# Kernel optimization log

Hardware: AMD Instinct MI355X
Metric: run time of the kernel (lower is better)

Reference implementation:

```python
import jax, jax.numpy as jnp
import numpy as np

B, N_PROP = 2, 512
C_FEAT, FH, FW = 256, 200, 200
NUM_CLASSES, NUM_STAGES = 81, 3
POOL, SR, SCALE = 7, 2, 0.25
IMG_H, IMG_W = 800.0, 800.0
FC_DIM = 1024
IN_DIM = C_FEAT * POOL * POOL
STDS = ((0.1, 0.1, 0.2, 0.2), (0.05, 0.05, 0.1, 0.1), (0.033, 0.033, 0.067, 0.067))
CLIP_VAL = float(np.log(1000.0 / 16))
SCORE_T, NMS_T, DETS, PRE_NMS = 0.05, 0.5, 100, 2048


def bilinear(f, y, x):
    # f: [C,H,W]; y,x: [M] sample coords (torchvision roi_align bilinear rules)
    H, W = f.shape[1], f.shape[2]
    valid = (y > -1.0) & (y < H) & (x > -1.0) & (x < W)
    y = jnp.clip(y, 0.0, H - 1.0)
    x = jnp.clip(x, 0.0, W - 1.0)
    y0 = jnp.floor(y).astype(jnp.int32)
    x0 = jnp.floor(x).astype(jnp.int32)
    y1 = jnp.minimum(y0 + 1, H - 1)
    x1 = jnp.minimum(x0 + 1, W - 1)
    ly, lx = y - y0, x - x0
    hy, hx = 1.0 - ly, 1.0 - lx
    v = (hy * hx) * f[:, y0, x0] + (hy * lx) * f[:, y0, x1] \
      + (ly * hx) * f[:, y1, x0] + (ly * lx) * f[:, y1, x1]
    return v * valid  # [C,M]


def roi_align(f, rois):
    # f: [C,H,W], rois: [N,4] image coords -> [N,C,POOL,POOL]
    b = rois * SCALE
    x1, y1, x2, y2 = b[:, 0], b[:, 1], b[:, 2], b[:, 3]
    rw = jnp.maximum(x2 - x1, 1.0)
    rh = jnp.maximum(y2 - y1, 1.0)
    bw, bh = rw / POOL, rh / POOL
    p = jnp.arange(POOL, dtype=f.dtype)
    s = (jnp.arange(SR, dtype=f.dtype) + 0.5) / SR
    gy = y1[:, None, None] + (p[None, :, None] + s[None, None, :]) * bh[:, None, None]  # [N,P,SR]
    gx = x1[:, None, None] + (p[None, :, None] + s[None, None, :]) * bw[:, None, None]
    n = rois.shape[0]
    yy = jnp.broadcast_to(gy[:, :, :, None, None], (n, POOL, SR, POOL, SR))
    xx = jnp.broadcast_to(gx[:, None, None, :, :], (n, POOL, SR, POOL, SR))
    vals = bilinear(f, yy.reshape(-1), xx.reshape(-1))  # [C, N*P*SR*P*SR]
    vals = vals.reshape(f.shape[0], n, POOL, SR, POOL, SR).mean(axis=(3, 5))
    return vals.transpose(1, 0, 2, 3)


def decode_clip(props, deltas, stds):
    px1, py1, px2, py2 = props[:, 0], props[:, 1], props[:, 2], props[:, 3]
    pw = jnp.maximum(px2 - px1, 1e-6)
    ph = jnp.maximum(py2 - py1, 1e-6)
    px = px1 + 0.5 * pw
    py = py1 + 0.5 * ph
    wx, wy, ww, wh = stds
    dx = deltas[:, 0] * wx
    dy = deltas[:, 1] * wy
    dw = jnp.minimum(deltas[:, 2] * ww, CLIP_VAL)
    dh = jnp.minimum(deltas[:, 3] * wh, CLIP_VAL)
    gx = dx * pw + px
    gy = dy * ph + py
    gw = jnp.exp(dw) * pw
    gh = jnp.exp(dh) * ph
    return jnp.stack([jnp.clip(gx - 0.5 * gw, 0.0, IMG_W),
                      jnp.clip(gy - 0.5 * gh, 0.0, IMG_H),
                      jnp.clip(gx + 0.5 * gw, 0.0, IMG_W),
                      jnp.clip(gy + 0.5 * gh, 0.0, IMG_H)], axis=1)


def box_iou(a, b):
    area_a = (a[:, 2] - a[:, 0]) * (a[:, 3] - a[:, 1])
    area_b = (b[:, 2] - b[:, 0]) * (b[:, 3] - b[:, 1])
    lt = jnp.maximum(a[:, None, :2], b[None, :, :2])
    rb = jnp.minimum(a[:, None, 2:], b[None, :, 2:])
    wh = jnp.maximum(rb - lt, 0.0)
    inter = wh[..., 0] * wh[..., 1]
    return inter / (area_a[:, None] + area_b[None, :] - inter + 1e-12)


def postprocess(boxes, probs):
    # boxes [N,4], probs [N,NUM_CLASSES] -> fixed-size padded detections
    n = boxes.shape[0]
    ws = boxes[:, 2] - boxes[:, 0]
    hs = boxes[:, 3] - boxes[:, 1]
    ok = (ws >= 1.0) & (hs >= 1.0)  # remove_small_boxes(min_size=1.0)
    fg = probs[:, 1:]               # drop background (class 0)
    sc = jnp.where((fg > SCORE_T) & ok[:, None], fg, -1.0).reshape(-1)  # [N*(C-1)]
    labels = jnp.broadcast_to(jnp.arange(1, NUM_CLASSES, dtype=jnp.int32)[None, :],
                              (n, NUM_CLASSES - 1)).reshape(-1)
    bflat = jnp.broadcast_to(boxes[:, None, :], (n, NUM_CLASSES - 1, 4)).reshape(-1, 4)
    vals, idx = jax.lax.top_k(sc, PRE_NMS)  # fixed-size candidate cap, sorted desc
    bsel = bflat[idx]
    lsel = labels[idx]
    # batched_nms trick: offset boxes per label so classes never overlap
    off = bsel + (lsel.astype(bsel.dtype) * (jnp.max(bsel) + 1.0))[:, None]
    iou = box_iou(off, off)
    valid = vals > 0.0
    ar = jnp.arange(PRE_NMS)
    def body(i, keep):
        sup = (iou[i] > NMS_T) & keep[i]
        return keep & ~(sup & (ar > i))
    keep = jax.lax.fori_loop(0, PRE_NMS, body, valid)
    order = jnp.argsort(jnp.where(keep, ar, PRE_NMS + ar))[:DETS]  # kept first, score order
    kv = keep[order]
    out_boxes = jnp.where(kv[:, None], bsel[order], 0.0)
    out_scores = jnp.where(kv, vals[order], 0.0)
    out_labels = jnp.where(kv, lsel[order], 0)
    return out_boxes, out_scores, out_labels


def cascade_forward(features, proposals, W1, b1, W2, b2, Wc, bc, Wr, br):
    cur = proposals  # [B,N,4]
    logits = None
    for s in range(NUM_STAGES):
        pooled = jax.vmap(roi_align)(features, cur)  # [B,N,C,P,P]
        x = pooled.reshape(B * N_PROP, IN_DIM)
        h = jax.nn.relu(x @ W1[s] + b1[s])
        h = jax.nn.relu(h @ W2[s] + b2[s])
        logits = h @ Wc[s] + bc[s]
        deltas = (h @ Wr[s] + br[s]).reshape(B, N_PROP, 4)
        stds = STDS[s]
        cur = jax.vmap(lambda p, d: decode_clip(p, d, stds))(cur, deltas)
    probs = jax.nn.softmax(logits, axis=-1).reshape(B, N_PROP, NUM_CLASSES)
    return jax.vmap(postprocess)(cur, probs)


def setup_inputs() -> dict:
    key = jax.random.key(0)
    ks = jax.random.split(key, 12)
    features = jax.random.normal(ks[0], (B, C_FEAT, FH, FW), jnp.float32)
    cx = jax.random.uniform(ks[1], (B, N_PROP), minval=0.0, maxval=IMG_W)
    cy = jax.random.uniform(ks[2], (B, N_PROP), minval=0.0, maxval=IMG_H)
    w = jax.random.uniform(ks[3], (B, N_PROP), minval=16.0, maxval=256.0)
    h = jax.random.uniform(ks[4], (B, N_PROP), minval=16.0, maxval=256.0)
    proposals = jnp.stack([jnp.clip(cx - w / 2, 0.0, IMG_W), jnp.clip(cy - h / 2, 0.0, IMG_H),
                           jnp.clip(cx + w / 2, 0.0, IMG_W), jnp.clip(cy + h / 2, 0.0, IMG_H)],
                          axis=-1)
    def lin(k, fan_in, shape):
        return jax.random.normal(k, shape, jnp.float32) / np.sqrt(fan_in).astype(np.float32)
    W1 = lin(ks[5], IN_DIM, (NUM_STAGES, IN_DIM, FC_DIM))
    W2 = lin(ks[6], FC_DIM, (NUM_STAGES, FC_DIM, FC_DIM))
    Wc = lin(ks[7], FC_DIM, (NUM_STAGES, FC_DIM, NUM_CLASSES))
    Wr = lin(ks[8], FC_DIM, (NUM_STAGES, FC_DIM, 4)) * 0.5
    b1 = jnp.zeros((NUM_STAGES, FC_DIM), jnp.float32)
    b2 = jnp.zeros((NUM_STAGES, FC_DIM), jnp.float32)
    bc = jnp.zeros((NUM_STAGES, NUM_CLASSES), jnp.float32)
    br = jnp.zeros((NUM_STAGES, 4), jnp.float32)
    return {"features": features, "proposals": proposals, "W1": W1, "b1": b1,
            "W2": W2, "b2": b2, "Wc": Wc, "bc": bc, "Wr": Wr, "br": br}


def reference(features, proposals, W1, b1, W2, b2, Wc, bc, Wr, br):
    return cascade_forward(features, proposals, W1, b1, W2, b2, Wc, bc, Wr, br)
```

## Files before the change

### kernel.cpp

```cpp
#include <hip/hip_runtime.h>
#include <float.h>
#include <math.h>

#define NB 2
#define NPROP 512
#define NROI 1024
#define CFEAT 256
#define FH 200
#define FW 200
#define HWSZ 40000
#define INDIM 12544
#define FCD 1024
#define NCLS 81
#define NCAND 40960
#define CAP 4096
#define NSEL 2048
#define DETS 100
#define CLIPV 4.135166556742356f

#define KKT1 392
#define KKT2 32
#define SPLITK 8

typedef __attribute__((ext_vector_type(8))) short short8v;
typedef __attribute__((ext_vector_type(8))) unsigned short ushort8v;
typedef __attribute__((ext_vector_type(4))) float float4v;

__device__ __forceinline__ unsigned short f2bf(float x) {
    unsigned u = __float_as_uint(x);
    unsigned r = (u + 0x7fffu + ((u >> 16) & 1u)) >> 16;
    return (unsigned short)r;
}
__device__ __forceinline__ float bf2f(unsigned short b) {
    return __uint_as_float(((unsigned)b) << 16);
}
__device__ __forceinline__ void split3(float x, unsigned short& h, unsigned short& m, unsigned short& l) {
    h = f2bf(x);
    float r1 = x - bf2f(h);
    m = f2bf(r1);
    float r2 = r1 - bf2f(m);
    l = f2bf(r2);
}

__device__ __forceinline__ void gload_lds16(const void* g, void* l) {
    __builtin_amdgcn_global_load_lds((const __attribute__((address_space(1))) unsigned int*)g,
                                     (__attribute__((address_space(3))) unsigned int*)l, 16, 0, 0);
}

__device__ __forceinline__ int swz8k(int o) {
    return o ^ ((((o >> 6) ^ (o >> 8)) & 3) << 4);
}

__global__ void zero_ints_k(int* p, int n) {
    int i = blockIdx.x * blockDim.x + threadIdx.x;
    if (i < n) p[i] = 0;
}

__global__ __launch_bounds__(256) void transpose_k(const float* __restrict__ in, float* __restrict__ out) {
    __shared__ float tile[32][33];
    int b = blockIdx.z;
    int hw0 = blockIdx.x * 32;
    int c0 = blockIdx.y * 32;
    int tx = threadIdx.x;
    int ty = threadIdx.y;
#pragma unroll
    for (int i = 0; i < 32; i += 8)
        tile[ty + i][tx] = in[((size_t)(b * CFEAT + c0 + ty + i)) * HWSZ + hw0 + tx];
    __syncthreads();
#pragma unroll
    for (int i = 0; i < 32; i += 8)
        out[((size_t)b * HWSZ + hw0 + ty + i) * CFEAT + c0 + tx] = tile[tx][ty + i];
}

template<bool TRANS>
__device__ __forceinline__ float bil_sample(const float* __restrict__ feat, int b, int c,
                                            float yy, float xx) {
    bool valid = (yy > -1.f) && (yy < (float)FH) && (xx > -1.f) && (xx < (float)FW);
    float yc = fminf(fmaxf(yy, 0.f), (float)(FH - 1));
    float xc = fminf(fmaxf(xx, 0.f), (float)(FW - 1));
    int y0 = (int)floorf(yc), x0 = (int)floorf(xc);
    int y1i = min(y0 + 1, FH - 1), x1i = min(x0 + 1, FW - 1);
    float ly = yc - (float)y0, lx = xc - (float)x0;
    float hy = 1.f - ly, hx = 1.f - lx;
    float v00, v01, v10, v11;
    if (TRANS) {
        const float* base = feat + (size_t)b * HWSZ * CFEAT;
        v00 = base[((size_t)(y0 * FW + x0)) * CFEAT + c];
        v01 = base[((size_t)(y0 * FW + x1i)) * CFEAT + c];
        v10 = base[((size_t)(y1i * FW + x0)) * CFEAT + c];
        v11 = base[((size_t)(y1i * FW + x1i)) * CFEAT + c];
    } else {
        const float* base = feat + ((size_t)(b * CFEAT + c)) * HWSZ;
        v00 = base[y0 * FW + x0];
        v01 = base[y0 * FW + x1i];
        v10 = base[y1i * FW + x0];
        v11 = base[y1i * FW + x1i];
    }
    float v = hy * hx * v00 + hy * lx * v01 + ly * hx * v10 + ly * lx * v11;
    return valid ? v : 0.f;
}

template<bool TRANS>
__global__ __launch_bounds__(256) void roi_k(const float* __restrict__ feat,
                                             const float* __restrict__ boxes,
                                             float* __restrict__ xout) {
    int pp = blockIdx.x, r = blockIdx.y, c = threadIdx.x;
    int b = r >> 9;
    const float* bx = boxes + (size_t)r * 4;
    float x1 = bx[0] * 0.25f, y1 = bx[1] * 0.25f, x2 = bx[2] * 0.25f, y2 = bx[3] * 0.25f;
    float rw = fmaxf(x2 - x1, 1.0f), rh = fmaxf(y2 - y1, 1.0f);
    float bw = rw / 7.0f, bh = rh / 7.0f;
    int py = pp / 7, px = pp % 7;
    float acc = 0.f;
#pragma unroll
    for (int sy = 0; sy < 2; ++sy)
#pragma unroll
        for (int sx = 0; sx < 2; ++sx)
            acc += bil_sample<TRANS>(feat, b, c,
                                     y1 + ((float)py + 0.25f + 0.5f * (float)sy) * bh,
                                     x1 + ((float)px + 0.25f + 0.5f * (float)sx) * bw);
    xout[(size_t)r * INDIM + pp * 256 + c] = acc * 0.25f;
}

__global__ __launch_bounds__(256) void roi_split4_k(const float* __restrict__ feat,
                                                    const float* __restrict__ boxes,
                                                    unsigned short* __restrict__ Ap) {
    int tid = threadIdx.x;
    int g = tid >> 7;
    int binhalf = (tid >> 6) & 1;
    int cl = tid & 63;
    int r = blockIdx.x * 2 + g;
    int b = r >> 9;
    const float* bx = boxes + (size_t)r * 4;
    float x1 = bx[0] * 0.25f, y1 = bx[1] * 0.25f, x2 = bx[2] * 0.25f, y2 = bx[3] * 0.25f;
    float rw = fmaxf(x2 - x1, 1.0f), rh = fmaxf(y2 - y1, 1.0f);
    float bw = rw / 7.0f, bh = rh / 7.0f;
    int mt = r >> 7, rr = r & 127;
    size_t pstr = (size_t)8 * KKT1 * 4096;
    const float* base = feat + (size_t)b * HWSZ * CFEAT;
    for (int pp = binhalf; pp < 49; pp += 2) {
        int py = pp / 7, px = pp % 7;
        float ax = 0.f, ay = 0.f, az = 0.f, aw = 0.f;
#pragma unroll
        for (int sy = 0; sy < 2; ++sy) {
#pragma unroll
            for (int sx = 0; sx < 2; ++sx) {
                float yy = y1 + ((float)py + 0.25f + 0.5f * (float)sy) * bh;
                float xx = x1 + ((float)px + 0.25f + 0.5f * (float)sx) * bw;
                bool valid = (yy > -1.f) && (yy < (float)FH) && (xx > -1.f) && (xx < (float)FW);
                float yc = fminf(fmaxf(yy, 0.f), (float)(FH - 1));
                float xc = fminf(fmaxf(xx, 0.f), (float)(FW - 1));
                int y0 = (int)floorf(yc), x0 = (int)floorf(xc);
                int y1i = min(y0 + 1, FH - 1), x1i = min(x0 + 1, FW - 1);
                float ly = yc - (float)y0, lx = xc - (float)x0;
                float hy = 1.f - ly, hx = 1.f - lx;
                float w00 = hy * hx, w01 = hy * lx, w10 = ly * hx, w11 = ly * lx;
                if (!valid) { w00 = w01 = w10 = w11 = 0.f; }
                float4 v00 = ((const float4*)(base + (size_t)(y0 * FW + x0) * CFEAT))[cl];
                float4 v01 = ((const float4*)(base + (size_t)(y0 * FW + x1i) * CFEAT))[cl];
                float4 v10 = ((const float4*)(base + (size_t)(y1i * FW + x0) * CFEAT))[cl];
                float4 v11 = ((const float4*)(base + (size_t)(y1i * FW + x1i) * CFEAT))[cl];
                ax += w00 * v00.x + w01 * v01.x + w10 * v10.x + w11 * v11.x;
                ay += w00 * v00.y + w01 * v01.y + w10 * v10.y + w11 * v11.y;
                az += w00 * v00.z + w01 * v01.z + w10 * v10.z + w11 * v11.z;
                aw += w00 * v00.w + w01 * v01.w + w10 * v10.w + w11 * v11.w;
            }
        }
        ax *= 0.25f; ay *= 0.25f; az *= 0.25f; aw *= 0.25f;
        ushort4 h4, m4, l4;
        split3(ax, h4.x, m4.x, l4.x);
        split3(ay, h4.y, m4.y, l4.y);
        split3(az, h4.z, m4.z, l4.z);
        split3(aw, h4.w, m4.w, l4.w);
        int k0 = pp * 256 + cl * 4;
        int kk = k0 >> 5;
        size_t tile = ((size_t)mt * KKT1 + kk) * 4096 + rr * 32 + (k0 & 31);
        *(ushort4*)&Ap[tile] = h4;
        *(ushort4*)&Ap[tile + pstr] = m4;
        *(ushort4*)&Ap[tile + 2 * pstr] = l4;
    }
}

template<bool PERM>
__global__ __launch_bounds__(256) void wsplit_k(const float* __restrict__ W,
                                                unsigned short* __restrict__ out, int kkT) {
    __shared__ float tf[32][132];
    int nt = blockIdx.x, kk = blockIdx.y;
    int t = threadIdx.x;
    int kloc = t >> 3;
    int f4 = t & 7;
    int krow;
    if (PERM) krow = ((kk & 7) * 32 + kloc) * 49 + (kk >> 3);
    else krow = kk * 32 + kloc;
    const float* src = W + (size_t)krow * 1024 + nt * 128;
#pragma unroll
    for (int q = 0; q < 4; ++q) {
        float4 v = *(const float4*)(src + (f4 + q * 8) * 4);
        *(float4*)&tf[kloc][(f4 + q * 8) * 4] = v;
    }
    __syncthreads();
    int r = t >> 1;
    size_t tileBase = ((size_t)nt * kkT + kk) * 4096;
    size_t pstr = (size_t)8 * kkT * 4096;
#pragma unroll
    for (int cc = 0; cc < 2; ++cc) {
        int c = (t & 1) * 2 + cc;
        ushort8v hv, mv, lv;
#pragma unroll
        for (int e = 0; e < 8; ++e) {
            unsigned short h, m, l;
            split3(tf[c * 8 + e][r], h, m, l);
            hv[e] = h; mv[e] = m; lv[e] = l;
        }
        size_t o = tileBase + r * 32 + c * 8;
        *(ushort8v*)&out[o] = hv;
        *(ushort8v*)&out[o + pstr] = mv;
        *(ushort8v*)&out[o + 2 * pstr] = lv;
    }
}

__global__ __launch_bounds__(256) void wsplit_head_k(const float* __restrict__ Wc,
                                                     const float* __restrict__ Wr,
                                                     unsigned short* __restrict__ out) {
    int kk = blockIdx.x, t = threadIdx.x;
    int r = t >> 1;
    int k0 = (t & 1) * 16;
    size_t pstr = (size_t)KKT2 * 4096;
    for (int e = 0; e < 16; ++e) {
        int k = k0 + e;
        int krow = kk * 32 + k;
        float v = 0.f;
        if (r < 81) v = Wc[(size_t)krow * 81 + r];
        else if (r < 85) v = Wr[(size_t)krow * 4 + (r - 81)];
        unsigned short h, m, l;
        split3(v, h, m, l);
        size_t o = (size_t)kk * 4096 + r * 32 + k;
        out[o] = h;
        out[o + pstr] = m;
        out[o + 2 * pstr] = l;
    }
}

#define TERM16(AF) { _Pragma("unroll") for (int i = 0; i < 4; ++i) _Pragma("unroll") \
    for (int j = 0; j < 4; ++j) acc[i][j] = __builtin_amdgcn_mfma_f32_16x16x32_bf16(AF[i], bf[j], acc[i][j], 0, 0, 0); }

__global__ __launch_bounds__(256) void gemm_mfma_k(const unsigned short* __restrict__ Ap,
                                                   const unsigned short* __restrict__ Bp,
                                                   float* __restrict__ partial,
                                                   int kkT, int kkPer, int NT, int N) {
    __shared__ unsigned short sA[3][4096];
    __shared__ unsigned short sB[3][4096];
    int tid = threadIdx.x;
    int phys = blockIdx.x;
    int logical = (phys & 7) * (gridDim.x >> 3) + (phys >> 3);
    int tpc = 8 * NT;
    int xy = logical % tpc;
    int ck = logical / tpc;
    int mt = xy & 7, nt = xy >> 3;
    int kk0 = ck * kkPer;
    size_t pstrA = (size_t)8 * kkT * 4096 * 2;
    size_t pstrB = (size_t)NT * kkT * 4096 * 2;
    const char* aBase = (const char*)(Ap + (size_t)mt * kkT * 4096);
    const char* bBase = (const char*)(Bp + (size_t)nt * kkT * 4096);

    float4v acc[4][4];
#pragma unroll
    for (int i = 0; i < 4; ++i)
#pragma unroll
        for (int j = 0; j < 4; ++j) acc[i][j] = (float4v){0.f, 0.f, 0.f, 0.f};

    int lane = tid & 63, wv = tid >> 6;
    int wr = wv >> 1, wc = wv & 1;
    int ln = lane & 15;
    int q = lane >> 4;
    int qs = (q ^ (ln ^ (ln >> 2))) & 3;
    int aoffE = (wr * 64 + ln) * 32 + qs * 8;
    int boffE = (wc * 64 + ln) * 32 + qs * 8;

    int o0 = tid * 16;
    int o1 = o0 + 4096;
    int s0 = swz8k(o0);
    int s1 = swz8k(o1);

    for (int kk = kk0; kk < kk0 + kkPer; ++kk) {
        const char* at = aBase + (size_t)kk * 8192;
        const char* bt = bBase + (size_t)kk * 8192;
#pragma unroll
        for (int p = 0; p < 3; ++p) {
            gload_lds16(at + (size_t)p * pstrA + s0, (char*)sA[p] + o0);
            gload_lds16(at + (size_t)p * pstrA + s1, (char*)sA[p] + o1);
            gload_lds16(bt + (size_t)p * pstrB + s0, (char*)sB[p] + o0);
            gload_lds16(bt + (size_t)p * pstrB + s1, (char*)sB[p] + o1);
        }
        __syncthreads();
        short8v af[3][4];
#pragma unroll
        for (int p = 0; p < 3; ++p)
#pragma unroll
            for (int f = 0; f < 4; ++f)
                af[p][f] = *(const short8v*)&sA[p][aoffE + f * 512];
        short8v bf[4];
#pragma unroll
        for (int f = 0; f < 4; ++f) bf[f] = *(const short8v*)&sB[0][boffE + f * 512];
        TERM16(af[0]); TERM16(af[1]); TERM16(af[2]);
#pragma unroll
        for (int f = 0; f < 4; ++f) bf[f] = *(const short8v*)&sB[1][boffE + f * 512];
        TERM16(af[0]); TERM16(af[1]);
#pragma unroll
        for (int f = 0; f < 4; ++f) bf[f] = *(const short8v*)&sB[2][boffE + f * 512];
        TERM16(af[0]);
        __syncthreads();
    }
    float* outp = partial + (size_t)ck * 1024 * N;
    int row0 = mt * 128 + wr * 64 + (lane >> 4) * 4;
    int col = nt * 128 + wc * 64 + ln;
#pragma unroll
    for (int i = 0; i < 4; ++i)
#pragma unroll
        for (int j = 0; j < 4; ++j)
#pragma unroll
            for (int qq = 0; qq < 4; ++qq)
                outp[(size_t)(row0 + i * 16 + qq) * N + col + j * 16] = acc[i][j][qq];
}

template<int NS>
__global__ void reduce8_k(const float* __restrict__ partial, const float* __restrict__ bias,
                          unsigned short* __restrict__ planes) {
    int i = blockIdx.x * 256 + threadIdx.x;
    float s = 0.f;
#pragma unroll
    for (int c = 0; c < NS; ++c) s += partial[((size_t)c << 20) + i];
    s += bias[i & 1023];
    s = fmaxf(s, 0.f);
    int m = i >> 10, n = i & 1023;
    int mt = m >> 7, rr = m & 127, kk = n >> 5;
    unsigned short h, mm_, l;
    split3(s, h, mm_, l);
    size_t tile = ((size_t)mt * KKT2 + kk) * 4096 + rr * 32 + (n & 31);
    size_t pstr = (size_t)8 * KKT2 * 4096;
    planes[tile] = h;
    planes[tile + pstr] = mm_;
    planes[tile + 2 * pstr] = l;
}

__global__ void head_fin_k(const float* __restrict__ partial, const float* __restrict__ bc,
                           const float* __restrict__ br, float* __restrict__ logits,
                           float* __restrict__ deltas, int write_logits) {
    int idx = blockIdx.x * 256 + threadIdx.x;
    if (idx >= 1024 * 85) return;
    int m = idx / 85, col = idx - m * 85;
    float s = 0.f;
#pragma unroll
    for (int c = 0; c < 8; ++c) s += partial[(size_t)c * 131072 + m * 128 + col];
    if (col < 81) {
        if (write_logits) logits[(size_t)m * NCLS + col] = s + bc[col];
    } else {
        deltas[(size_t)m * 4 + (col - 81)] = s + br[col - 81];
    }
}

template<bool PERM>
__global__ __launch_bounds__(256) void gemm_k(const float* __restrict__ A,
                                              const float* __restrict__ Bm,
                                              float* __restrict__ partial,
                                              int K_total, int Kchunk) {
    const int M = 1024, N = 1024;
    __shared__ float As[2][16][128];
    __shared__ float Bs[2][16][64];
    int tid = threadIdx.x;
    int mb = blockIdx.x & 7;
    int nb = blockIdx.x >> 3;
    int ck = blockIdx.y;
    int k0 = ck * Kchunk;
    int am = tid >> 1;
    int ak = (tid & 1) * 8;
    int bk = tid >> 4;
    int bn = (tid & 15) * 4;
    int ty = tid >> 4, tx = tid & 15;
    const float* Aptr = A + (size_t)(mb * 128 + am) * K_total + k0 + ak;

    float acc[8][4];
#pragma unroll
    for (int i = 0; i < 8; ++i)
#pragma unroll
        for (int j = 0; j < 4; ++j) acc[i][j] = 0.f;

    auto bRowPtr = [&](int kk) -> const float* {
        int row = PERM ? ((kk & 255) * 49 + (kk >> 8)) : kk;
        return Bm + (size_t)row * N + nb * 64 + bn;
    };

    int T = Kchunk / 16;
    float4 a0 = *(const float4*)(Aptr);
    float4 a1 = *(const float4*)(Aptr + 4);
    float4 b0 = *(const float4*)bRowPtr(k0 + bk);
    As[0][ak + 0][am] = a0.x; As[0][ak + 1][am] = a0.y; As[0][ak + 2][am] = a0.z; As[0][ak + 3][am] = a0.w;
    As[0][ak + 4][am] = a1.x; As[0][ak + 5][am] = a1.y; As[0][ak + 6][am] = a1.z; As[0][ak + 7][am] = a1.w;
    *(float4*)&Bs[0][bk][bn] = b0;
    __syncthreads();

    int p = 0;
    for (int t = 0; t < T; ++t) {
        if (t + 1 < T) {
            a0 = *(const float4*)(Aptr + (t + 1) * 16);
            a1 = *(const float4*)(Aptr + (t + 1) * 16 + 4);
            b0 = *(const float4*)bRowPtr(k0 + (t + 1) * 16 + bk);
        }
#pragma unroll
        for (int k = 0; k < 16; ++k) {
            float4 av0 = *(const float4*)&As[p][k][ty * 8];
            float4 av1 = *(const float4*)&As[p][k][ty * 8 + 4];
            float4 bv = *(const float4*)&Bs[p][k][tx * 4];
            float ar[8] = {av0.x, av0.y, av0.z, av0.w, av1.x, av1.y, av1.z, av1.w};
            float br_[4] = {bv.x, bv.y, bv.z, bv.w};
#pragma unroll
            for (int i = 0; i < 8; ++i)
#pragma unroll
                for (int j = 0; j < 4; ++j) acc[i][j] = fmaf(ar[i], br_[j], acc[i][j]);
        }
        if (t + 1 < T) {
            __syncthreads();
            int qb = 1 - p;
            As[qb][ak + 0][am] = a0.x; As[qb][ak + 1][am] = a0.y; As[qb][ak + 2][am] = a0.z; As[qb][ak + 3][am] = a0.w;
            As[qb][ak + 4][am] = a1.x; As[qb][ak + 5][am] = a1.y; As[qb][ak + 6][am] = a1.z; As[qb][ak + 7][am] = a1.w;
            *(float4*)&Bs[qb][bk][bn] = b0;
            __syncthreads();
            p = qb;
        }
    }
    float* out = partial + ((size_t)ck * M + mb * 128 + ty * 8) * N + nb * 64 + tx * 4;
#pragma unroll
    for (int i = 0; i < 8; ++i) {
        float4 v = make_float4(acc[i][0], acc[i][1], acc[i][2], acc[i][3]);
        *(float4*)(out + (size_t)i * N) = v;
    }
}

__global__ void reduce4_k(const float* __restrict__ partial, const float* __restrict__ bias,
                          float* __restrict__ out) {
    const int MN = 1024 * 1024;
    int i = blockIdx.x * 256 + threadIdx.x;
    if (i >= MN) return;
    float s = partial[i] + partial[(size_t)MN + i] + partial[(size_t)2 * MN + i] + partial[(size_t)3 * MN + i];
    s += bias[i & 1023];
    out[i] = fmaxf(s, 0.f);
}

__global__ __launch_bounds__(128) void head_k(const float* __restrict__ h,
                                              const float* __restrict__ Wc, const float* __restrict__ bc,
                                              const float* __restrict__ Wr, const float* __restrict__ br,
                                              float* __restrict__ logits, float* __restrict__ deltas,
                                              int write_logits) {
    __shared__ float hs[1024];
    int m = blockIdx.x;
    int tid = threadIdx.x;
    const float4* hp = (const float4*)(h + (size_t)m * 1024);
    ((float4*)hs)[tid] = hp[tid];
    ((float4*)hs)[tid + 128] = hp[tid + 128];
    __syncthreads();
    int j = tid;
    if (j < 85) {
        bool is_cls = j < 81;
        const float* Wp = is_cls ? Wc : Wr;
        int stride = is_cls ? 81 : 4;
        int col = is_cls ? j : j - 81;
        float s0 = 0.f, s1 = 0.f, s2 = 0.f, s3 = 0.f;
        for (int k = 0; k < 1024; k += 4) {
            s0 = fmaf(hs[k + 0], Wp[(k + 0) * stride + col], s0);
            s1 = fmaf(hs[k + 1], Wp[(k + 1) * stride + col], s1);
            s2 = fmaf(hs[k + 2], Wp[(k + 2) * stride + col], s2);
            s3 = fmaf(hs[k + 3], Wp[(k + 3) * stride + col], s3);
        }
        float s = (s0 + s1) + (s2 + s3);
        if (is_cls) {
            if (write_logits) logits[(size_t)m * NCLS + col] = s + bc[col];
        } else {
            deltas[(size_t)m * 4 + col] = s + br[col];
        }
    }
}

__global__ void decode_k(const float* __restrict__ prev, const float* __restrict__ deltas,
                         float* __restrict__ nxt, float wx, float wy, float ww, float wh) {
    int r = blockIdx.x * 256 + threadIdx.x;
    if (r >= NROI) return;
    const float* p = prev + (size_t)r * 4;
    const float* d = deltas + (size_t)r * 4;
    float px1 = p[0], py1 = p[1], px2 = p[2], py2 = p[3];
    float pw = fmaxf(px2 - px1, 1e-6f), ph = fmaxf(py2 - py1, 1e-6f);
    float pcx = px1 + 0.5f * pw, pcy = py1 + 0.5f * ph;
    float dx = d[0] * wx, dy = d[1] * wy;
    float dw = fminf(d[2] * ww, CLIPV);
    float dh = fminf(d[3] * wh, CLIPV);
    float gx = dx * pw + pcx, gy = dy * ph + pcy;
    float gw = expf(dw) * pw, gh = expf(dh) * ph;
    nxt[(size_t)r * 4 + 0] = fminf(fmaxf(gx - 0.5f * gw, 0.f), 800.f);
    nxt[(size_t)r * 4 + 1] = fminf(fmaxf(gy - 0.5f * gh, 0.f), 800.f);
    nxt[(size_t)r * 4 + 2] = fminf(fmaxf(gx + 0.5f * gw, 0.f), 800.f);
    nxt[(size_t)r * 4 + 3] = fminf(fmaxf(gy + 0.5f * gh, 0.f), 800.f);
}

__global__ __launch_bounds__(128) void softmax_k(const float* __restrict__ logits, float* __restrict__ probs) {
    __shared__ float red[128];
    int m = blockIdx.x;
    int tid = threadIdx.x;
    float v = (tid < NCLS) ? logits[(size_t)m * NCLS + tid] : -FLT_MAX;
    red[tid] = v;
    __syncthreads();
    for (int o = 64; o; o >>= 1) {
        if (tid < o) red[tid] = fmaxf(red[tid], red[tid + o]);
        __syncthreads();
    }
    float mx = red[0];
    __syncthreads();
    float e = (tid < NCLS) ? expf(v - mx) : 0.f;
    red[tid] = e;
    __syncthreads();
    for (int o = 64; o; o >>= 1) {
        if (tid < o) red[tid] += red[tid + o];
        __syncthreads();
    }
    float s = red[0];
    if (tid < NCLS) probs[(size_t)m * NCLS + tid] = e / s;
}

__global__ void build_scores_k(const float* __restrict__ probs, const float* __restrict__ boxes,
                               float* __restrict__ sc, int* __restrict__ vcount) {
    int f = blockIdx.x * 256 + threadIdx.x;
    if (f >= NB * NCAND) return;
    int b = f / NCAND, ff = f % NCAND;
    int rr = ff / 80, cls = ff % 80 + 1;
    int row = b * NPROP + rr;
    const float* bx = boxes + (size_t)row * 4;
    bool ok = (bx[2] - bx[0] >= 1.f) && (bx[3] - bx[1] >= 1.f);
    float p = probs[(size_t)row * NCLS + cls];
    float s = (p > 0.05f && ok) ? p : -1.0f;
    sc[f] = s;
    if (s > 0.f) atomicAdd(&vcount[b], 1);
}

__global__ __launch_bounds__(1024) void find_pivot_k(const float* __restrict__ sc,
                                                     const int* __restrict__ vcount,
                                                     float* __restrict__ pivot) {
    int b = blockIdx.x;
    const float* s = sc + (size_t)b * NCAND;
    __shared__ int tot;
    int V = vcount[b];
    if (V <= CAP) {
        if (threadIdx.x == 0) pivot[b] = 0.f;
        return;
    }
    unsigned u = 0;
    for (int bit = 30; bit >= 0; --bit) {
        unsigned cand = u | (1u << bit);
        float cf = __uint_as_float(cand);
        if (threadIdx.x == 0) tot = 0;
        __syncthreads();
        int cnt = 0;
        for (int i = threadIdx.x; i < NCAND; i += 1024) cnt += (s[i] >= cf) ? 1 : 0;
        for (int o = 32; o; o >>= 1) cnt += __shfl_down(cnt, o);
        if ((threadIdx.x & 63) == 0) atomicAdd(&tot, cnt);
        __syncthreads();
        if (tot >= NSEL) u = cand;
        __syncthreads();
    }
    if (threadIdx.x == 0) pivot[b] = __uint_as_float(u);
}

__global__ void compact_k(const float* __restrict__ sc, const float* __restrict__ pivot,
                          float* __restrict__ ckey, int* __restrict__ cidx, int* __restrict__ ccount) {
    int f = blockIdx.x * 256 + threadIdx.x;
    if (f >= NB * NCAND) return;
    int b = f / NCAND, ff = f % NCAND;
    float s = sc[f];
    float pv = pivot[b];
    if (s > 0.f && s >= pv) {
        int slot = atomicAdd(&ccount[b], 1);
        if (slot < CAP) {
            ckey[(size_t)b * CAP + slot] = s;
            cidx[(size_t)b * CAP + slot] = ff;
        }
    }
}

__global__ __launch_bounds__(1024) void sort_select_k(const float* __restrict__ ckey,
                                                      const int* __restrict__ cidx,
                                                      const int* __restrict__ ccount,
                                                      const float* __restrict__ boxes,
                                                      float* __restrict__ selb, float* __restrict__ seloff,
                                                      float* __restrict__ selsc, int* __restrict__ sellab,
                                                      unsigned long long* __restrict__ vmask) {
    int b = blockIdx.x;
    __shared__ float ks[CAP];
    __shared__ int is[CAP];
    __shared__ float rmax[1024];
    int cnt = min(ccount[b], CAP);
    for (int i = threadIdx.x; i < CAP; i += 1024) {
        if (i < cnt) {
            ks[i] = ckey[(size_t)b * CAP + i];
            is[i] = cidx[(size_t)b * CAP + i];
        } else {
            ks[i] = -FLT_MAX;
            is[i] = 0x7FFFFFFF;
        }
    }
    __syncthreads();
    for (int k = 2; k <= CAP; k <<= 1) {
        for (int j = k >> 1; j > 0; j >>= 1) {
            for (int t = threadIdx.x; t < CAP; t += 1024) {
                int l = t ^ j;
                if (l > t) {
                    bool up = ((t & k) == 0);
                    float a = ks[t], bb = ks[l];
                    int ia = is[t], ib = is[l];
                    bool a_first = (a > bb) || (a == bb && ia < ib);
                    bool doswap = up ? !a_first : a_first;
                    if (doswap) {
                        ks[t] = bb; ks[l] = a;
                        is[t] = ib; is[l] = ia;
                    }
                }
            }
            __syncthreads();
        }
    }
    float lm = -FLT_MAX;
    for (int i = threadIdx.x; i < NSEL; i += 1024) {
        if (ks[i] > 0.f) {
            const float* bb = boxes + (size_t)(b * NPROP + is[i] / 80) * 4;
            lm = fmaxf(lm, fmaxf(fmaxf(bb[0], bb[1]), fmaxf(bb[2], bb[3])));
        }
    }
    rmax[threadIdx.x] = lm;
    __syncthreads();
    for (int o = 512; o; o >>= 1) {
        if (threadIdx.x < o) rmax[threadIdx.x] = fmaxf(rmax[threadIdx.x], rmax[threadIdx.x + o]);
        __syncthreads();
    }
    float maxb = (rmax[0] > -FLT_MAX) ? rmax[0] : 0.f;
    __syncthreads();
    for (int pass = 0; pass < 2; ++pass) {
        int i = pass * 1024 + threadIdx.x;
        bool v = ks[i] > 0.f;
        int idx = is[i];
        int rr = idx / 80;
        int cls = idx % 80 + 1;
        float b0 = 0.f, b1 = 0.f, b2 = 0.f, b3 = 0.f, offv = 0.f;
        if (v) {
            const float* bb = boxes + (size_t)(b * NPROP + rr) * 4;
            b0 = bb[0]; b1 = bb[1]; b2 = bb[2]; b3 = bb[3];
            offv = (maxb + 1.f) * (float)cls;
        }
        float* sb = selb + ((size_t)b * NSEL + i) * 4;
        sb[0] = b0; sb[1] = b1; sb[2] = b2; sb[3] = b3;
        float* so = seloff + ((size_t)b * NSEL + i) * 4;
        so[0] = b0 + offv; so[1] = b1 + offv; so[2] = b2 + offv; so[3] = b3 + offv;
        selsc[(size_t)b * NSEL + i] = v ? ks[i] : 0.f;
        sellab[(size_t)b * NSEL + i] = cls;
        unsigned long long m = __ballot(v);
        if ((threadIdx.x & 63) == 0) vmask[b * 32 + pass * 16 + (threadIdx.x >> 6)] = m;
    }
}

__global__ __launch_bounds__(256) void sup_k(const float* __restrict__ seloff,
                                             const float* __restrict__ selsc,
                                             unsigned long long* __restrict__ sup) {
    int b = blockIdx.y;
    int wave = threadIdx.x >> 6;
    int lane = threadIdx.x & 63;
    int pair = blockIdx.x * 4 + wave;
    int i = pair >> 5;
    int w = pair & 31;
    int j = w * 64 + lane;
    unsigned long long m = 0;
    if (w >= (i >> 6) && selsc[(size_t)b * NSEL + i] > 0.f) {
        const float* oi = seloff + ((size_t)b * NSEL + i) * 4;
        const float* oj = seloff + ((size_t)b * NSEL + j) * 4;
        float ax1 = oi[0], ay1 = oi[1], ax2 = oi[2], ay2 = oi[3];
        float bx1 = oj[0], by1 = oj[1], bx2 = oj[2], by2 = oj[3];
        float areaA = (ax2 - ax1) * (ay2 - ay1);
        float areaB = (bx2 - bx1) * (by2 - by1);
        float ltx = fmaxf(ax1, bx1), lty = fmaxf(ay1, by1);
        float rbx = fminf(ax2, bx2), rby = fminf(ay2, by2);
        float iw = fmaxf(rbx - ltx, 0.f), ih = fmaxf(rby - lty, 0.f);
        float inter = iw * ih;
        float iou = inter / (areaA + areaB - inter + 1e-12f);
        m = __ballot(iou > 0.5f);
    }
    if (lane == 0) sup[((size_t)b * NSEL + i) * 32 + w] = m;
}

__global__ __launch_bounds__(256) void nms_scan_k(const unsigned long long* __restrict__ vmask,
                                                  const unsigned long long* __restrict__ sup,
                                                  const float* __restrict__ selb,
                                                  const float* __restrict__ selsc,
                                                  const int* __restrict__ sellab,
                                                  float* __restrict__ out) {
    int b = blockIdx.x;
    __shared__ unsigned long long keepw[32];
    __shared__ int pref[33];
    int tid = threadIdx.x;
    if (tid < 64) {
        int lane = tid;
        unsigned long long kw = (lane < 32) ? vmask[b * 32 + lane] : 0ull;
        const unsigned long long* supB = sup + (size_t)b * NSEL * 32;
        int kept = 0;
        for (int w = 0; w < 32; ++w) {
            unsigned long long cur = __shfl(kw, w);
            if (cur) {
                unsigned long long R = supB[(size_t)(w * 64 + lane) * 32 + w];
                for (int b0 = 0; b0 < 64; b0 += 8) {
                    unsigned long long r0 = __shfl(R, b0 + 0);
                    unsigned long long r1 = __shfl(R, b0 + 1);
                    unsigned long long r2 = __shfl(R, b0 + 2);
                    unsigned long long r3 = __shfl(R, b0 + 3);
                    unsigned long long r4 = __shfl(R, b0 + 4);
                    unsigned long long r5 = __shfl(R, b0 + 5);
                    unsigned long long r6 = __shfl(R, b0 + 6);
                    unsigned long long r7 = __shfl(R, b0 + 7);
                    unsigned long long hi;
#define NMS_STEP(rr_, dd_) { int bb = b0 + dd_; \
                    hi = (bb == 63) ? 0ull : (~0ull << (bb + 1)); \
                    cur &= ~((0ull - ((cur >> bb) & 1ull)) & rr_ & hi); }
                    NMS_STEP(r0, 0) NMS_STEP(r1, 1) NMS_STEP(r2, 2) NMS_STEP(r3, 3)
                    NMS_STEP(r4, 4) NMS_STEP(r5, 5) NMS_STEP(r6, 6) NMS_STEP(r7, 7)
#undef NMS_STEP
                }
                kept += __popcll(cur);
                if (lane == w) kw = cur;
                if (kept >= DETS) break;
                int v = lane & 31;
                int h = lane >> 5;
                unsigned long long acc = 0;
                const unsigned long long* rowb = supB + (size_t)(w * 64 + h) * 32 + v;
#pragma unroll 8
                for (int t = 0; t < 32; ++t) {
                    unsigned long long msk = 0ull - ((cur >> (h + 2 * t)) & 1ull);
                    acc |= rowb[(size_t)(2 * t) * 32] & msk;
                }
                acc |= __shfl_xor(acc, 32);
                if (lane < 32 && lane > w) kw &= ~acc;
            }
        }
        if (lane < 32) keepw[lane] = kw;
    }
    __syncthreads();
    if (tid == 0) {
        int s = 0;
        for (int w = 0; w < 32; ++w) { pref[w] = s; s += __popcll(keepw[w]); }
        pref[32] = s;
    }
    __syncthreads();
    for (int i = tid; i < 600; i += 256) {
        if (i < 400) out[b * 400 + i] = 0.f;
        else if (i < 500) out[800 + b * 100 + (i - 400)] = 0.f;
        else out[1000 + b * 100 + (i - 500)] = 0.f;
    }
    __syncthreads();
    for (int e = tid; e < NSEL; e += 256) {
        int w = e >> 6;
        unsigned long long kw = keepw[w];
        if ((kw >> (e & 63)) & 1ull) {
            int rank = pref[w] + __popcll(kw & ((1ull << (e & 63)) - 1ull));
            if (rank < DETS) {
                const float* sb = selb + ((size_t)b * NSEL + e) * 4;
                out[b * 400 + rank * 4 + 0] = sb[0];
                out[b * 400 + rank * 4 + 1] = sb[1];
                out[b * 400 + rank * 4 + 2] = sb[2];
                out[b * 400 + rank * 4 + 3] = sb[3];
                out[800 + b * 100 + rank] = selsc[(size_t)b * NSEL + e];
                out[1000 + b * 100 + rank] = (float)sellab[(size_t)b * NSEL + e];
            }
        }
    }
}

extern "C" void kernel_launch(void* const* d_in, const int* in_sizes, int n_in,
                              void* d_out, int out_size, void* d_ws, size_t ws_size,
                              hipStream_t stream) {
    const float* features = (const float*)d_in[0];
    const float* proposals = (const float*)d_in[1];
    const float* W1 = (const float*)d_in[2];
    const float* b1 = (const float*)d_in[3];
    const float* W2 = (const float*)d_in[4];
    const float* b2 = (const float*)d_in[5];
    const float* Wc = (const float*)d_in[6];
    const float* bc = (const float*)d_in[7];
    const float* Wr = (const float*)d_in[8];
    const float* br = (const float*)d_in[9];

    char* ws = (char*)d_ws;
    size_t off = 0;
    auto alloc = [&](size_t bytes) -> void* {
        void* p = ws + off;
        off += (bytes + 255) & ~(size_t)255;
        return p;
    };

    float* logits = (float*)alloc((size_t)NROI * NCLS * 4);
    float* probs = (float*)alloc((size_t)NROI * NCLS * 4);
    float* deltas = (float*)alloc((size_t)NROI * 4 * 4);
    float* cur1 = (float*)alloc((size_t)NROI * 4 * 4);
    float* cur2 = (float*)alloc((size_t)NROI * 4 * 4);
    float* cur3 = (float*)alloc((size_t)NROI * 4 * 4);
    float* sc = (float*)alloc((size_t)NB * NCAND * 4);
    float* ckey = (float*)alloc((size_t)NB * CAP * 4);
    int* cidx = (int*)alloc((size_t)NB * CAP * 4);
    int* counters = (int*)alloc(256);
    float* pivot = (float*)(counters + 4);
    float* selb = (float*)alloc((size_t)NB * NSEL * 4 * 4);
    float* seloff = (float*)alloc((size_t)NB * NSEL * 4 * 4);
    float* selsc = (float*)alloc((size_t)NB * NSEL * 4);
    int* sellab = (int*)alloc((size_t)NB * NSEL * 4);
    unsigned long long* vmask = (unsigned long long*)alloc((size_t)NB * 32 * 8);
    unsigned long long* sup = (unsigned long long*)alloc((size_t)NB * NSEL * 32 * 8);

    const float stds[3][4] = {{0.1f, 0.1f, 0.2f, 0.2f},
                              {0.05f, 0.05f, 0.1f, 0.1f},
                              {0.033f, 0.033f, 0.067f, 0.067f}};
    float* curbufs[3] = {cur1, cur2, cur3};
    const float* curp = proposals;

    size_t planes1 = (size_t)3 * 8 * KKT1 * 4096 * 2;
    size_t planes2 = (size_t)3 * 8 * KKT2 * 4096 * 2;
    size_t planesH = (size_t)3 * 1 * KKT2 * 4096 * 2;
    size_t mfma_need = planes1 * 2 + planes2 * 3 + planesH +
                       (size_t)SPLITK * (1 << 20) * 4 +
                       (size_t)NB * HWSZ * CFEAT * 4 + 65536;

    zero_ints_k<<<1, 64, 0, stream>>>(counters, 4);

    if (off + mfma_need <= ws_size) {
        unsigned short* Ap1 = (unsigned short*)alloc(planes1);
        unsigned short* Bp1 = (unsigned short*)alloc(planes1);
        unsigned short* h1p = (unsigned short*)alloc(planes2);
        unsigned short* W2Tp = (unsigned short*)alloc(planes2);
        unsigned short* h2p = (unsigned short*)alloc(planes2);
        unsigned short* Whp = (unsigned short*)alloc(planesH);
        float* partial = (float*)alloc((size_t)SPLITK * (1 << 20) * 4);
        float* featT = (float*)alloc((size_t)NB * HWSZ * CFEAT * 4);

        transpose_k<<<dim3(1250, 8, 2), dim3(32, 8), 0, stream>>>(features, featT);

        for (int s = 0; s < 3; ++s) {
            roi_split4_k<<<dim3(NROI / 2), 256, 0, stream>>>(featT, curp, Ap1);
            wsplit_k<true><<<dim3(8, KKT1), 256, 0, stream>>>(W1 + (size_t)s * INDIM * FCD, Bp1, KKT1);
            gemm_mfma_k<<<dim3(64 * SPLITK), 256, 0, stream>>>(Ap1, Bp1, partial, KKT1, KKT1 / SPLITK, 8, 1024);
            reduce8_k<SPLITK><<<4096, 256, 0, stream>>>(partial, b1 + s * FCD, h1p);
            wsplit_k<false><<<dim3(8, KKT2), 256, 0, stream>>>(W2 + (size_t)s * FCD * FCD, W2Tp, KKT2);
            gemm_mfma_k<<<dim3(512), 256, 0, stream>>>(h1p, W2Tp, partial, KKT2, 4, 8, 1024);
            reduce8_k<8><<<4096, 256, 0, stream>>>(partial, b2 + s * FCD, h2p);
            wsplit_head_k<<<dim3(KKT2), 256, 0, stream>>>(Wc + (size_t)s * FCD * NCLS,
                                                          Wr + (size_t)s * FCD * 4, Whp);
            gemm_mfma_k<<<dim3(64), 256, 0, stream>>>(h2p, Whp, partial, KKT2, 4, 1, 128);
            head_fin_k<<<dim3(340), 256, 0, stream>>>(partial, bc + s * NCLS, br + s * 4,
                                                      logits, deltas, (s == 2) ? 1 : 0);
            decode_k<<<4, 256, 0, stream>>>(curp, deltas, curbufs[s],
                                            stds[s][0], stds[s][1], stds[s][2], stds[s][3]);
            curp = curbufs[s];
        }
    } else {
        float* x = (float*)alloc((size_t)NROI * INDIM * 4);
        float* partial = (float*)alloc((size_t)4 * 1024 * 1024 * 4);
        float* h1 = (float*)alloc((size_t)NROI * FCD * 4);
        float* h2 = (float*)alloc((size_t)NROI * FCD * 4);
        float* featT = (float*)alloc((size_t)NB * HWSZ * CFEAT * 4);
        bool use_trans = (off <= ws_size);

        if (use_trans)
            transpose_k<<<dim3(1250, 8, 2), dim3(32, 8), 0, stream>>>(features, featT);

        for (int s = 0; s < 3; ++s) {
            if (use_trans)
                roi_k<true><<<dim3(49, 1024), 256, 0, stream>>>(featT, curp, x);
            else
                roi_k<false><<<dim3(49, 1024), 256, 0, stream>>>(features, curp, x);
            gemm_k<true><<<dim3(128, 4), 256, 0, stream>>>(x, W1 + (size_t)s * INDIM * FCD, partial, INDIM, 3136);
            reduce4_k<<<4096, 256, 0, stream>>>(partial, b1 + s * FCD, h1);
            gemm_k<false><<<dim3(128, 4), 256, 0, stream>>>(h1, W2 + (size_t)s * FCD * FCD, partial, FCD, 256);
            reduce4_k<<<4096, 256, 0, stream>>>(partial, b2 + s * FCD, h2);
            head_k<<<1024, 128, 0, stream>>>(h2, Wc + (size_t)s * FCD * NCLS, bc + s * NCLS,
                                             Wr + (size_t)s * FCD * 4, br + s * 4,
                                             logits, deltas, (s == 2) ? 1 : 0);
            decode_k<<<4, 256, 0, stream>>>(curp, deltas, curbufs[s],
                                            stds[s][0], stds[s][1], stds[s][2], stds[s][3]);
            curp = curbufs[s];
        }
    }

    softmax_k<<<1024, 128, 0, stream>>>(logits, probs);
    build_scores_k<<<320, 256, 0, stream>>>(probs, curp, sc, counters);
    find_pivot_k<<<2, 1024, 0, stream>>>(sc, counters, pivot);
    compact_k<<<320, 256, 0, stream>>>(sc, pivot, ckey, cidx, counters + 2);
    sort_select_k<<<2, 1024, 0, stream>>>(ckey, cidx, counters + 2, curp, selb, seloff, selsc, sellab, vmask);
    sup_k<<<dim3(16384, 2), 256, 0, stream>>>(seloff, selsc, sup);
    nms_scan_k<<<2, 256, 0, stream>>>(vmask, sup, selb, selsc, sellab, (float*)d_out);
}
```

Before: 1.083 ms.

## Double-buffer LDS tiles in split-K MFMA GEMM to overlap loads with compute

Doubles the shared-memory staging buffers for the A and B bf16 planes so the next K tile's global-to-LDS loads are issued before the current tile's MFMAs run. Manual vmcnt waits and raw barriers plus scheduling barriers replace __syncthreads, so memory latency can overlap with compute. LDS use per block doubles to 96KB, which can lower occupancy. The hand-counted vmcnt(12) has to match the number of outstanding loads per stage exactly.

```diff
diff --git a/kernel.cpp b/kernel.cpp
--- a/kernel.cpp
+++ b/kernel.cpp
@@ -248,8 +248,8 @@
                                                    const unsigned short* __restrict__ Bp,
                                                    float* __restrict__ partial,
                                                    int kkT, int kkPer, int NT, int N) {
-    __shared__ unsigned short sA[3][4096];
-    __shared__ unsigned short sB[3][4096];
+    __shared__ unsigned short sA[2][3][4096];
+    __shared__ unsigned short sB[2][3][4096];
     int tid = threadIdx.x;
     int phys = blockIdx.x;
     int logical = (phys & 7) * (gridDim.x >> 3) + (phys >> 3);
@@ -282,34 +282,47 @@
     int s0 = swz8k(o0);
     int s1 = swz8k(o1);
 
-    for (int kk = kk0; kk < kk0 + kkPer; ++kk) {
+    auto stage = [&](int buf, int kk) {
         const char* at = aBase + (size_t)kk * 8192;
         const char* bt = bBase + (size_t)kk * 8192;
 #pragma unroll
         for (int p = 0; p < 3; ++p) {
-            gload_lds16(at + (size_t)p * pstrA + s0, (char*)sA[p] + o0);
-            gload_lds16(at + (size_t)p * pstrA + s1, (char*)sA[p] + o1);
-            gload_lds16(bt + (size_t)p * pstrB + s0, (char*)sB[p] + o0);
-            gload_lds16(bt + (size_t)p * pstrB + s1, (char*)sB[p] + o1);
-        }
-        __syncthreads();
+            gload_lds16(at + (size_t)p * pstrA + s0, (char*)sA[buf][p] + o0);
+            gload_lds16(at + (size_t)p * pstrA + s1, (char*)sA[buf][p] + o1);
+            gload_lds16(bt + (size_t)p * pstrB + s0, (char*)sB[buf][p] + o0);
+            gload_lds16(bt + (size_t)p * pstrB + s1, (char*)sB[buf][p] + o1);
+        }
+    };
+
+    stage(0, kk0);
+    for (int it = 0; it < kkPer; ++it) {
+        int cur = it & 1;
+        if (it + 1 < kkPer) {
+            stage(cur ^ 1, kk0 + it + 1);
+            asm volatile("s_waitcnt vmcnt(12)" ::: "memory");
+        } else {
+            asm volatile("s_waitcnt vmcnt(0)" ::: "memory");
+        }
+        __builtin_amdgcn_s_barrier();
+        __builtin_amdgcn_sched_barrier(0);
         short8v af[3][4];
 #pragma unroll
         for (int p = 0; p < 3; ++p)
 #pragma unroll
             for (int f = 0; f < 4; ++f)
-                af[p][f] = *(const short8v*)&sA[p][aoffE + f * 512];
+                af[p][f] = *(const short8v*)&sA[cur][p][aoffE + f * 512];
         short8v bf[4];
 #pragma unroll
-        for (int f = 0; f < 4; ++f) bf[f] = *(const short8v*)&sB[0][boffE + f * 512];
+        for (int f = 0; f < 4; ++f) bf[f] = *(const short8v*)&sB[cur][0][boffE + f * 512];
         TERM16(af[0]); TERM16(af[1]); TERM16(af[2]);
 #pragma unroll
-        for (int f = 0; f < 4; ++f) bf[f] = *(const short8v*)&sB[1][boffE + f * 512];
+        for (int f = 0; f < 4; ++f) bf[f] = *(const short8v*)&sB[cur][1][boffE + f * 512];
         TERM16(af[0]); TERM16(af[1]);
 #pragma unroll
-        for (int f = 0; f < 4; ++f) bf[f] = *(const short8v*)&sB[2][boffE + f * 512];
+        for (int f = 0; f < 4; ++f) bf[f] = *(const short8v*)&sB[cur][2][boffE + f * 512];
         TERM16(af[0]);
-        __syncthreads();
+        __builtin_amdgcn_sched_barrier(0);
+        __builtin_amdgcn_s_barrier();
     }
     float* outp = partial + (size_t)ck * 1024 * N;
     int row0 = mt * 128 + wr * 64 + (lane >> 4) * 4;
```

After: 1.301 ms. 20.1% more time.
